# Optimization experiments

Measured on AMD Instinct MI355X. Metric: run time of the kernel, lower is better.

The kernel has to match this reference:

```python
import jax, jax.numpy as jnp
import numpy as np

N, D, H, E, K = 8192, 512, 2048, 8, 2  # tokens, input/output dim, hidden, experts, top-k
EPS = float(np.finfo(np.float64).eps)   # np.finfo(float).eps used by SparseDispatcher
NOISE_EPS = 1e-2                        # standard noisy-top-k gating epsilon


def setup_inputs() -> dict:
    key = jax.random.key(0)
    ks = jax.random.split(key, 8)
    s = 0.02  # weight scale to keep exp() in combine numerically sane
    return {
        "x": jax.random.normal(ks[0], (N, D), jnp.float32),
        "gate_feat": jax.random.normal(ks[1], (N, 2 * D), jnp.float32),
        "noise": jax.random.normal(ks[2], (N, E), jnp.float32),
        "w_gate": jax.random.normal(ks[3], (2 * D, E), jnp.float32) * s,
        "w_noise": jax.random.normal(ks[4], (2 * D, E), jnp.float32) * s,
        "fc1_w": jax.random.normal(ks[5], (E, H, D), jnp.float32) * s,
        "fc1_b": jnp.zeros((E, H), jnp.float32),
        "fc2_w": jax.random.normal(ks[6], (E, D, H), jnp.float32) * s,
        "fc2_b": jnp.zeros((E, D), jnp.float32),
    }


def reference(x, gate_feat, noise, w_gate, w_noise, fc1_w, fc1_b, fc2_w, fc2_b):
    # --- noisy top-k gating ---
    clean_logits = gate_feat @ w_gate                               # [N, E]
    noise_stddev = jax.nn.softplus(gate_feat @ w_noise) + NOISE_EPS  # [N, E]
    logits = clean_logits + noise * noise_stddev                    # randn_like * stddev
    top_vals, top_idx = jax.lax.top_k(logits, K + 1)                # top k+1 as in Shazeer gating
    top_k_gates = jax.nn.softmax(top_vals[:, :K], axis=-1)          # softmax over top-k logits
    gates = jnp.zeros_like(logits).at[jnp.arange(N)[:, None], top_idx[:, :K]].set(top_k_gates)

    # --- per-expert MLP (grouped GEMM; dense-masked form, math-equal to sparse dispatch
    # since zero-gate contributions vanish in the weighted combine) ---
    h = jax.nn.gelu(jnp.einsum('nd,ehd->enh', x, fc1_w) + fc1_b[:, None, :],
                    approximate=False)                              # torch nn.GELU = exact erf
    expert_out = jnp.einsum('enh,eoh->eno', h, fc2_w) + fc2_b[:, None, :]  # [E, N, D]

    # --- SparseDispatcher.combine: exp, gate-weight, scatter-add, eps-fill, log ---
    combined = jnp.einsum('ne,eno->no', gates, jnp.exp(expert_out))  # [N, D]
    combined = jnp.where(combined == 0, EPS, combined)
    return jnp.log(combined)
```

## Files before the change

kernel.cpp:

```cpp
#include <hip/hip_runtime.h>
#include <hip/hip_bf16.h>

#define NTOK 8192
#define DIM  512
#define HID  2048
#define NEXP 8
#define GFD  1024
#define NPAIR (NTOK*2)
#define EPSD 2.220446049250313e-16f

typedef __bf16 bf16;
typedef __bf16 bf16x4 __attribute__((ext_vector_type(4)));
typedef __bf16 bf16x8 __attribute__((ext_vector_type(8)));
typedef float  f32x4  __attribute__((ext_vector_type(4)));

__device__ __forceinline__ void cvt4(const float* __restrict__ src,
                                     bf16* __restrict__ dst, int i) {
    float4 v = ((const float4*)src)[i];
    bf16x4 o = { (bf16)v.x, (bf16)v.y, (bf16)v.z, (bf16)v.w };
    ((bf16x4*)dst)[i] = o;
}

__global__ __launch_bounds__(256) void convert_kernel(
    const float* __restrict__ x, const float* __restrict__ w1,
    const float* __restrict__ w2,
    bf16* __restrict__ xo, bf16* __restrict__ w1o, bf16* __restrict__ w2o)
{
    int tid = blockIdx.x * 256 + threadIdx.x;
    int stride = gridDim.x * 256;
    for (int i = tid; i < NTOK*DIM/4; i += stride)      cvt4(x,  xo,  i);
    for (int i = tid; i < NEXP*HID*DIM/4; i += stride)  cvt4(w1, w1o, i);
    for (int i = tid; i < NEXP*DIM*HID/4; i += stride)  cvt4(w2, w2o, i);
}

__global__ __launch_bounds__(256) void gate_gemm_kernel(
    const float* __restrict__ gf, const float* __restrict__ wg,
    const float* __restrict__ wn, float* __restrict__ partial)
{
    const int bt = blockIdx.x;
    const int bd = blockIdx.y;
    const int tid = threadIdx.x;

    __shared__ float sgf[128*129];
    __shared__ float sw[128][16];

    #pragma unroll
    for (int i = 0; i < 4; ++i) {
        int idx = i*256 + tid;
        sw[idx>>3][idx&7]     = wg[bd*1024 + idx];
        sw[idx>>3][8+(idx&7)] = wn[bd*1024 + idx];
    }
    const float4* gf4 = (const float4*)gf;
    #pragma unroll
    for (int i = 0; i < 16; ++i) {
        int c = i*256 + tid;
        int row = c >> 5, c4 = c & 31;
        float4 v = gf4[(size_t)(bt*128+row)*(GFD/4) + bd*32 + c4];
        float* dst = sgf + row*129 + c4*4;
        dst[0]=v.x; dst[1]=v.y; dst[2]=v.z; dst[3]=v.w;
    }
    __syncthreads();

    const int og = tid >> 6;
    const int lane = tid & 63;
    const int t0 = lane*2, t1 = t0+1;
    float a0=0,a1=0,a2=0,a3=0, b0=0,b1=0,b2=0,b3=0;
    #pragma unroll 4
    for (int dd = 0; dd < 128; ++dd) {
        float f0 = sgf[t0*129+dd];
        float f1 = sgf[t1*129+dd];
        float4 w = *(const float4*)&sw[dd][og*4];
        a0 += f0*w.x; a1 += f0*w.y; a2 += f0*w.z; a3 += f0*w.w;
        b0 += f1*w.x; b1 += f1*w.y; b2 += f1*w.z; b3 += f1*w.w;
    }
    size_t pbase = ((size_t)bd*NTOK + bt*128)*16 + og*4;
    *(float4*)&partial[pbase + (size_t)t0*16] = make_float4(a0,a1,a2,a3);
    *(float4*)&partial[pbase + (size_t)t1*16] = make_float4(b0,b1,b2,b3);
}

__global__ __launch_bounds__(256) void finalize_kernel(
    const float* __restrict__ partial, const float* __restrict__ noise,
    int* __restrict__ tok_e, float* __restrict__ tok_g, int* __restrict__ counts)
{
    __shared__ int hist[8];
    int tid = threadIdx.x;
    if (tid < 8) hist[tid] = 0;
    __syncthreads();
    int n = blockIdx.x*256 + tid;

    float lg[16];
    #pragma unroll
    for (int k = 0; k < 16; ++k) lg[k] = 0.f;
    #pragma unroll
    for (int j = 0; j < 8; ++j) {
        const float4* p = (const float4*)(partial + ((size_t)j*NTOK + n)*16);
        float4 q0 = p[0], q1 = p[1], q2 = p[2], q3 = p[3];
        lg[0]+=q0.x; lg[1]+=q0.y; lg[2]+=q0.z; lg[3]+=q0.w;
        lg[4]+=q1.x; lg[5]+=q1.y; lg[6]+=q1.z; lg[7]+=q1.w;
        lg[8]+=q2.x; lg[9]+=q2.y; lg[10]+=q2.z; lg[11]+=q2.w;
        lg[12]+=q3.x; lg[13]+=q3.y; lg[14]+=q3.z; lg[15]+=q3.w;
    }
    float v0=-1e30f, v1=-1e30f; int i0=0, i1=0;
    #pragma unroll
    for (int e = 0; e < 8; ++e) {
        float xn = lg[8+e];
        float sp = fmaxf(xn, 0.f) + log1pf(expf(-fabsf(xn)));
        float l = lg[e] + noise[(size_t)n*NEXP+e] * (sp + 1e-2f);
        if (l > v0)      { v1=v0; i1=i0; v0=l; i0=e; }
        else if (l > v1) { v1=l; i1=e; }
    }
    float g1 = expf(v1 - v0);
    float s  = 1.0f + g1;
    tok_e[n] = i0 | (i1 << 8);
    tok_g[2*n]   = 1.0f / s;
    tok_g[2*n+1] = g1 / s;
    atomicAdd(&hist[i0], 1);
    atomicAdd(&hist[i1], 1);
    __syncthreads();
    if (tid < 8) atomicAdd(&counts[tid], hist[tid]);
}

__global__ void scan_kernel(const int* __restrict__ counts,
                            int* __restrict__ offsets, int* __restrict__ cursors)
{
    if (threadIdx.x == 0) {
        int s = 0;
        for (int e = 0; e < NEXP; ++e) { offsets[e] = s; cursors[e] = s; s += counts[e]; }
        offsets[NEXP] = s;
    }
}

__global__ __launch_bounds__(256) void dispatch_kernel(
    const int* __restrict__ tok_e, const float* __restrict__ tok_g,
    int* __restrict__ cursors, int* __restrict__ pair_token, float* __restrict__ pair_gate,
    int* __restrict__ slot0, int* __restrict__ slot1)
{
    __shared__ int hist[8];
    __shared__ int base[8];
    int tid = threadIdx.x;
    if (tid < 8) hist[tid] = 0;
    __syncthreads();
    int n = blockIdx.x*256 + tid;
    int ee = tok_e[n];
    int e0 = ee & 255, e1 = (ee >> 8) & 255;
    atomicAdd(&hist[e0], 1);
    atomicAdd(&hist[e1], 1);
    __syncthreads();
    if (tid < 8) base[tid] = atomicAdd(&cursors[tid], hist[tid]);
    __syncthreads();
    int s0 = atomicAdd(&base[e0], 1);
    pair_token[s0] = n; pair_gate[s0] = tok_g[2*n];
    slot0[n] = s0;
    int s1 = atomicAdd(&base[e1], 1);
    pair_token[s1] = n; pair_gate[s1] = tok_g[2*n+1];
    slot1[n] = s1;
}

#define GLL16(gsrc, ldst) \
    __builtin_amdgcn_global_load_lds( \
        (__attribute__((address_space(1))) void*)(gsrc), \
        (__attribute__((address_space(3))) void*)(ldst), 16, 0, 0)

__global__ __launch_bounds__(256) void gemm1_kernel(
    const bf16* __restrict__ xb, const bf16* __restrict__ w1b,
    const float* __restrict__ fc1b,
    const int* __restrict__ pair_token, const int* __restrict__ offsets,
    bf16* __restrict__ hbuf)
{
    const int nt = blockIdx.x;
    const int mt = blockIdx.y;
    const int e  = blockIdx.z;
    const int seg0 = offsets[e], seg1 = offsets[e+1];
    const int cnt = seg1 - seg0;
    const int mbase = mt * 128;
    if (mbase >= cnt) return;

    __shared__ bf16 ldsA[128*64];
    __shared__ bf16 ldsB[128*64];

    const int tid = threadIdx.x;
    const int wid = tid >> 6;
    const int lane = tid & 63;
    const int wr = wid >> 1, wc = wid & 1;

    const bf16* srcA[4];
    const bf16* srcB[4];
    #pragma unroll
    for (int i = 0; i < 4; ++i) {
        int c = wid*256 + i*64 + lane;
        int r = c >> 3, c16 = c & 7;
        int sw = (c16 ^ (r & 7)) * 8;
        int p = seg0 + mbase + r;
        if (p > seg1 - 1) p = seg1 - 1;
        srcA[i] = xb + (size_t)pair_token[p] * DIM + sw;
        srcB[i] = w1b + ((size_t)e*HID + nt*128 + r) * DIM + sw;
    }

    f32x4 acc[4][4] = {};

    for (int kk = 0; kk < DIM; kk += 64) {
        #pragma unroll
        for (int i = 0; i < 4; ++i) {
            GLL16(srcA[i] + kk, (char*)ldsA + wid*4096 + i*1024);
            GLL16(srcB[i] + kk, (char*)ldsB + wid*4096 + i*1024);
        }
        __syncthreads();
        #pragma unroll
        for (int ks = 0; ks < 2; ++ks) {
            bf16x8 av[4], bv[4];
            #pragma unroll
            for (int m = 0; m < 4; ++m) {
                int row = wr*64 + m*16 + (lane & 15);
                int sw = (ks*4 + (lane >> 4)) ^ (row & 7);
                av[m] = *(const bf16x8*)(ldsA + row*64 + sw*8);
            }
            #pragma unroll
            for (int n = 0; n < 4; ++n) {
                int row = wc*64 + n*16 + (lane & 15);
                int sw = (ks*4 + (lane >> 4)) ^ (row & 7);
                bv[n] = *(const bf16x8*)(ldsB + row*64 + sw*8);
            }
            #pragma unroll
            for (int m = 0; m < 4; ++m)
                #pragma unroll
                for (int n = 0; n < 4; ++n)
                    acc[m][n] = __builtin_amdgcn_mfma_f32_16x16x32_bf16(
                        av[m], bv[n], acc[m][n], 0, 0, 0);
        }
        __syncthreads();
    }

    #pragma unroll
    for (int m = 0; m < 4; ++m) {
        #pragma unroll
        for (int jj = 0; jj < 4; ++jj) {
            int rt = wr*64 + m*16 + (lane >> 4)*4 + jj;
            int row = mbase + rt;
            if (row < cnt) {
                size_t hrow = (size_t)(seg0 + row) * HID;
                #pragma unroll
                for (int n = 0; n < 4; ++n) {
                    int col = nt*128 + wc*64 + n*16 + (lane & 15);
                    float v = acc[m][n][jj] + fc1b[e*HID + col];
                    float g = 0.5f * v * (1.0f + erff(v * 0.70710678118654752f));
                    hbuf[hrow + col] = (bf16)g;
                }
            }
        }
    }
}

__global__ __launch_bounds__(256) void gemm2_kernel(
    const bf16* __restrict__ hbuf, const bf16* __restrict__ w2b,
    const float* __restrict__ fc2b,
    const float* __restrict__ pair_gate,
    const int* __restrict__ offsets, bf16* __restrict__ pout)
{
    const int nt = blockIdx.x;
    const int mt = blockIdx.y;
    const int e  = blockIdx.z;
    const int seg0 = offsets[e], seg1 = offsets[e+1];
    const int cnt = seg1 - seg0;
    const int mbase = mt * 128;
    if (mbase >= cnt) return;

    __shared__ bf16 ldsA[128*64];
    __shared__ bf16 ldsB[128*64];

    const int tid = threadIdx.x;
    const int wid = tid >> 6;
    const int lane = tid & 63;
    const int wr = wid >> 1, wc = wid & 1;

    const bf16* srcA[4];
    const bf16* srcB[4];
    #pragma unroll
    for (int i = 0; i < 4; ++i) {
        int c = wid*256 + i*64 + lane;
        int r = c >> 3, c16 = c & 7;
        int sw = (c16 ^ (r & 7)) * 8;
        int p = seg0 + mbase + r;
        if (p > seg1 - 1) p = seg1 - 1;
        srcA[i] = hbuf + (size_t)p * HID + sw;
        srcB[i] = w2b + ((size_t)e*DIM + nt*128 + r) * HID + sw;
    }

    f32x4 acc[4][4] = {};

    for (int kk = 0; kk < HID; kk += 64) {
        #pragma unroll
        for (int i = 0; i < 4; ++i) {
            GLL16(srcA[i] + kk, (char*)ldsA + wid*4096 + i*1024);
            GLL16(srcB[i] + kk, (char*)ldsB + wid*4096 + i*1024);
        }
        __syncthreads();
        #pragma unroll
        for (int ks = 0; ks < 2; ++ks) {
            bf16x8 av[4], bv[4];
            #pragma unroll
            for (int m = 0; m < 4; ++m) {
                int row = wr*64 + m*16 + (lane & 15);
                int sw = (ks*4 + (lane >> 4)) ^ (row & 7);
                av[m] = *(const bf16x8*)(ldsA + row*64 + sw*8);
            }
            #pragma unroll
            for (int n = 0; n < 4; ++n) {
                int row = wc*64 + n*16 + (lane & 15);
                int sw = (ks*4 + (lane >> 4)) ^ (row & 7);
                bv[n] = *(const bf16x8*)(ldsB + row*64 + sw*8);
            }
            #pragma unroll
            for (int m = 0; m < 4; ++m)
                #pragma unroll
                for (int n = 0; n < 4; ++n)
                    acc[m][n] = __builtin_amdgcn_mfma_f32_16x16x32_bf16(
                        av[m], bv[n], acc[m][n], 0, 0, 0);
        }
        __syncthreads();
    }

    #pragma unroll
    for (int m = 0; m < 4; ++m) {
        #pragma unroll
        for (int jj = 0; jj < 4; ++jj) {
            int rt = wr*64 + m*16 + (lane >> 4)*4 + jj;
            int row = mbase + rt;
            if (row < cnt) {
                int p = seg0 + row;
                float gate = pair_gate[p];
                bf16* prow = pout + (size_t)p * DIM;
                #pragma unroll
                for (int n = 0; n < 4; ++n) {
                    int col = nt*128 + wc*64 + n*16 + (lane & 15);
                    float v = acc[m][n][jj] + fc2b[e*DIM + col];
                    prow[col] = (bf16)(gate * expf(v));
                }
            }
        }
    }
}

__global__ __launch_bounds__(256) void combine_kernel(
    const bf16* __restrict__ pout, const int* __restrict__ slot0,
    const int* __restrict__ slot1, float* __restrict__ out)
{
    const int wid = threadIdx.x >> 6;
    const int lane = threadIdx.x & 63;
    const int n = blockIdx.x*4 + wid;
    const int s0 = slot0[n], s1 = slot1[n];
    bf16x8 a = ((const bf16x8*)(pout + (size_t)s0 * DIM))[lane];
    bf16x8 b = ((const bf16x8*)(pout + (size_t)s1 * DIM))[lane];
    float4 r0, r1;
    float* orow = out + (size_t)n * DIM + lane*8;
    float c;
    c = (float)a[0] + (float)b[0]; r0.x = logf(c == 0.f ? EPSD : c);
    c = (float)a[1] + (float)b[1]; r0.y = logf(c == 0.f ? EPSD : c);
    c = (float)a[2] + (float)b[2]; r0.z = logf(c == 0.f ? EPSD : c);
    c = (float)a[3] + (float)b[3]; r0.w = logf(c == 0.f ? EPSD : c);
    c = (float)a[4] + (float)b[4]; r1.x = logf(c == 0.f ? EPSD : c);
    c = (float)a[5] + (float)b[5]; r1.y = logf(c == 0.f ? EPSD : c);
    c = (float)a[6] + (float)b[6]; r1.z = logf(c == 0.f ? EPSD : c);
    c = (float)a[7] + (float)b[7]; r1.w = logf(c == 0.f ? EPSD : c);
    ((float4*)orow)[0] = r0;
    ((float4*)orow)[1] = r1;
}

extern "C" void kernel_launch(void* const* d_in, const int* in_sizes, int n_in,
                              void* d_out, int out_size, void* d_ws, size_t ws_size,
                              hipStream_t stream)
{
    const float* x     = (const float*)d_in[0];
    const float* gf    = (const float*)d_in[1];
    const float* noise = (const float*)d_in[2];
    const float* wg    = (const float*)d_in[3];
    const float* wn    = (const float*)d_in[4];
    const float* fc1w  = (const float*)d_in[5];
    const float* fc1b  = (const float*)d_in[6];
    const float* fc2w  = (const float*)d_in[7];
    const float* fc2b  = (const float*)d_in[8];
    float* out = (float*)d_out;

    char* ws = (char*)d_ws;
    size_t off = 0;
    bf16* xb  = (bf16*)(ws + off); off += (size_t)NTOK*DIM*2;
    bf16* w1b = (bf16*)(ws + off); off += (size_t)NEXP*HID*DIM*2;
    bf16* w2b = (bf16*)(ws + off); off += (size_t)NEXP*DIM*HID*2;
    bf16* hb  = (bf16*)(ws + off); off += (size_t)NPAIR*HID*2;
    int*   pair_token = (int*)  (ws + off); off += (size_t)NPAIR*4;
    float* pair_gate  = (float*)(ws + off); off += (size_t)NPAIR*4;
    int*   tok_e      = (int*)  (ws + off); off += (size_t)NTOK*4;
    float* tok_g      = (float*)(ws + off); off += (size_t)NTOK*2*4;
    int*   slot0      = (int*)  (ws + off); off += (size_t)NTOK*4;
    int*   slot1      = (int*)  (ws + off); off += (size_t)NTOK*4;
    int*   counts     = (int*)  (ws + off); off += 64;
    int*   offsets    = (int*)  (ws + off); off += 64;
    int*   cursors    = (int*)  (ws + off); off += 64;
    if (ws_size < off) return;

    float* partial = (float*)hb;
    bf16* pout = (bf16*)ws;

    hipMemsetAsync(counts, 0, 32, stream);
    convert_kernel<<<2048, 256, 0, stream>>>(x, fc1w, fc2w, xb, w1b, w2b);
    gate_gemm_kernel<<<dim3(64, 8), 256, 0, stream>>>(gf, wg, wn, partial);
    finalize_kernel<<<NTOK/256, 256, 0, stream>>>(partial, noise, tok_e, tok_g, counts);
    scan_kernel<<<1, 64, 0, stream>>>(counts, offsets, cursors);
    dispatch_kernel<<<NTOK/256, 256, 0, stream>>>(tok_e, tok_g, cursors,
                                                  pair_token, pair_gate, slot0, slot1);
    gemm1_kernel<<<dim3(16, 64, 8), 256, 0, stream>>>(xb, w1b, fc1b, pair_token, offsets, hb);
    gemm2_kernel<<<dim3(4, 64, 8), 256, 0, stream>>>(hb, w2b, fc2b, pair_gate, offsets, pout);
    combine_kernel<<<NTOK/4, 256, 0, stream>>>(pout, slot0, slot1, out);
}
```

Before: 237.0 us.

## Use compact tile list for grouped GEMMs and widen gemm1 tiles to 128x256

The scan kernel now builds a compact list of (expert, m-tile) pairs, so both GEMMs launch a grid sized to the real tile count instead of 64 m-tiles per expert, most of which exited at once. gemm1 moves to 512 threads with a 128x256 output tile, so each staged A tile is reused across twice as many columns. MFMA sections are also wrapped in s_setprio. The risks are more LDS per block and lower occupancy in gemm1, and MAXTILES=136 is a fixed upper bound on the tile count.

Measured after the change: 197.5 us (median of 3 runs). 1.2x faster.

```diff
diff --git a/kernel.cpp b/kernel.cpp
--- a/kernel.cpp
+++ b/kernel.cpp
@@ -8,6 +8,7 @@
 #define GFD  1024
 #define NPAIR (NTOK*2)
 #define EPSD 2.220446049250313e-16f
+#define MAXTILES 136
 
 typedef __bf16 bf16;
 typedef __bf16 bf16x4 __attribute__((ext_vector_type(4)));
@@ -121,12 +122,19 @@
 }
 
 __global__ void scan_kernel(const int* __restrict__ counts,
-                            int* __restrict__ offsets, int* __restrict__ cursors)
+                            int* __restrict__ offsets, int* __restrict__ cursors,
+                            int* __restrict__ tlist, int* __restrict__ ntiles)
 {
     if (threadIdx.x == 0) {
-        int s = 0;
-        for (int e = 0; e < NEXP; ++e) { offsets[e] = s; cursors[e] = s; s += counts[e]; }
+        int s = 0, nt = 0;
+        for (int e = 0; e < NEXP; ++e) {
+            offsets[e] = s; cursors[e] = s;
+            int c = counts[e];
+            for (int mt = 0; mt*128 < c; ++mt) tlist[nt++] = e | (mt << 8);
+            s += c;
+        }
         offsets[NEXP] = s;
+        ntiles[0] = nt;
     }
 }
 
@@ -161,49 +169,59 @@
         (__attribute__((address_space(1))) void*)(gsrc), \
         (__attribute__((address_space(3))) void*)(ldst), 16, 0, 0)
 
-__global__ __launch_bounds__(256) void gemm1_kernel(
+__global__ __launch_bounds__(512) void gemm1_kernel(
     const bf16* __restrict__ xb, const bf16* __restrict__ w1b,
     const float* __restrict__ fc1b,
     const int* __restrict__ pair_token, const int* __restrict__ offsets,
+    const int* __restrict__ tlist, const int* __restrict__ ntiles,
     bf16* __restrict__ hbuf)
 {
-    const int nt = blockIdx.x;
-    const int mt = blockIdx.y;
-    const int e  = blockIdx.z;
+    const int ntp = blockIdx.x;
+    const int tix = blockIdx.y;
+    if (tix >= ntiles[0]) return;
+    const int code = tlist[tix];
+    const int e  = code & 255;
+    const int mt = code >> 8;
     const int seg0 = offsets[e], seg1 = offsets[e+1];
     const int cnt = seg1 - seg0;
     const int mbase = mt * 128;
-    if (mbase >= cnt) return;
 
     __shared__ bf16 ldsA[128*64];
-    __shared__ bf16 ldsB[128*64];
+    __shared__ bf16 ldsB[256*64];
 
     const int tid = threadIdx.x;
     const int wid = tid >> 6;
     const int lane = tid & 63;
-    const int wr = wid >> 1, wc = wid & 1;
-
-    const bf16* srcA[4];
+    const int wr = wid >> 2, wc = wid & 3;
+
+    const bf16* srcA[2];
     const bf16* srcB[4];
     #pragma unroll
-    for (int i = 0; i < 4; ++i) {
-        int c = wid*256 + i*64 + lane;
+    for (int i = 0; i < 2; ++i) {
+        int c = i*512 + tid;
         int r = c >> 3, c16 = c & 7;
         int sw = (c16 ^ (r & 7)) * 8;
         int p = seg0 + mbase + r;
         if (p > seg1 - 1) p = seg1 - 1;
         srcA[i] = xb + (size_t)pair_token[p] * DIM + sw;
-        srcB[i] = w1b + ((size_t)e*HID + nt*128 + r) * DIM + sw;
+    }
+    #pragma unroll
+    for (int i = 0; i < 4; ++i) {
+        int c = i*512 + tid;
+        int r = c >> 3, c16 = c & 7;
+        int sw = (c16 ^ (r & 7)) * 8;
+        srcB[i] = w1b + ((size_t)e*HID + ntp*256 + r) * DIM + sw;
     }
 
     f32x4 acc[4][4] = {};
 
     for (int kk = 0; kk < DIM; kk += 64) {
         #pragma unroll
-        for (int i = 0; i < 4; ++i) {
-            GLL16(srcA[i] + kk, (char*)ldsA + wid*4096 + i*1024);
-            GLL16(srcB[i] + kk, (char*)ldsB + wid*4096 + i*1024);
-        }
+        for (int i = 0; i < 2; ++i)
+            GLL16(srcA[i] + kk, (char*)ldsA + i*8192 + tid*16);
+        #pragma unroll
+        for (int i = 0; i < 4; ++i)
+            GLL16(srcB[i] + kk, (char*)ldsB + i*8192 + tid*16);
         __syncthreads();
         #pragma unroll
         for (int ks = 0; ks < 2; ++ks) {
@@ -220,12 +238,14 @@
                 int sw = (ks*4 + (lane >> 4)) ^ (row & 7);
                 bv[n] = *(const bf16x8*)(ldsB + row*64 + sw*8);
             }
+            __builtin_amdgcn_s_setprio(1);
             #pragma unroll
             for (int m = 0; m < 4; ++m)
                 #pragma unroll
                 for (int n = 0; n < 4; ++n)
                     acc[m][n] = __builtin_amdgcn_mfma_f32_16x16x32_bf16(
                         av[m], bv[n], acc[m][n], 0, 0, 0);
+            __builtin_amdgcn_s_setprio(0);
         }
         __syncthreads();
     }
@@ -240,7 +260,7 @@
                 size_t hrow = (size_t)(seg0 + row) * HID;
                 #pragma unroll
                 for (int n = 0; n < 4; ++n) {
-                    int col = nt*128 + wc*64 + n*16 + (lane & 15);
+                    int col = ntp*256 + wc*64 + n*16 + (lane & 15);
                     float v = acc[m][n][jj] + fc1b[e*HID + col];
                     float g = 0.5f * v * (1.0f + erff(v * 0.70710678118654752f));
                     hbuf[hrow + col] = (bf16)g;
@@ -254,15 +274,19 @@
     const bf16* __restrict__ hbuf, const bf16* __restrict__ w2b,
     const float* __restrict__ fc2b,
     const float* __restrict__ pair_gate,
-    const int* __restrict__ offsets, bf16* __restrict__ pout)
+    const int* __restrict__ offsets,
+    const int* __restrict__ tlist, const int* __restrict__ ntiles,
+    bf16* __restrict__ pout)
 {
     const int nt = blockIdx.x;
-    const int mt = blockIdx.y;
-    const int e  = blockIdx.z;
+    const int tix = blockIdx.y;
+    if (tix >= ntiles[0]) return;
+    const int code = tlist[tix];
+    const int e  = code & 255;
+    const int mt = code >> 8;
     const int seg0 = offsets[e], seg1 = offsets[e+1];
     const int cnt = seg1 - seg0;
     const int mbase = mt * 128;
-    if (mbase >= cnt) return;
 
     __shared__ bf16 ldsA[128*64];
     __shared__ bf16 ldsB[128*64];
@@ -309,12 +333,14 @@
                 int sw = (ks*4 + (lane >> 4)) ^ (row & 7);
                 bv[n] = *(const bf16x8*)(ldsB + row*64 + sw*8);
             }
+            __builtin_amdgcn_s_setprio(1);
             #pragma unroll
             for (int m = 0; m < 4; ++m)
                 #pragma unroll
                 for (int n = 0; n < 4; ++n)
                     acc[m][n] = __builtin_amdgcn_mfma_f32_16x16x32_bf16(
                         av[m], bv[n], acc[m][n], 0, 0, 0);
+            __builtin_amdgcn_s_setprio(0);
         }
         __syncthreads();
     }
@@ -395,6 +421,8 @@
     int*   counts     = (int*)  (ws + off); off += 64;
     int*   offsets    = (int*)  (ws + off); off += 64;
     int*   cursors    = (int*)  (ws + off); off += 64;
+    int*   tlist      = (int*)  (ws + off); off += MAXTILES*4;
+    int*   ntiles     = (int*)  (ws + off); off += 64;
     if (ws_size < off) return;
 
     float* partial = (float*)hb;
@@ -404,10 +432,12 @@
     convert_kernel<<<2048, 256, 0, stream>>>(x, fc1w, fc2w, xb, w1b, w2b);
     gate_gemm_kernel<<<dim3(64, 8), 256, 0, stream>>>(gf, wg, wn, partial);
     finalize_kernel<<<NTOK/256, 256, 0, stream>>>(partial, noise, tok_e, tok_g, counts);
-    scan_kernel<<<1, 64, 0, stream>>>(counts, offsets, cursors);
+    scan_kernel<<<1, 64, 0, stream>>>(counts, offsets, cursors, tlist, ntiles);
     dispatch_kernel<<<NTOK/256, 256, 0, stream>>>(tok_e, tok_g, cursors,
                                                   pair_token, pair_gate, slot0, slot1);
-    gemm1_kernel<<<dim3(16, 64, 8), 256, 0, stream>>>(xb, w1b, fc1b, pair_token, offsets, hb);
-    gemm2_kernel<<<dim3(4, 64, 8), 256, 0, stream>>>(hb, w2b, fc2b, pair_gate, offsets, pout);
+    gemm1_kernel<<<dim3(8, MAXTILES), 512, 0, stream>>>(xb, w1b, fc1b, pair_token, offsets,
+                                                        tlist, ntiles, hb);
+    gemm2_kernel<<<dim3(4, MAXTILES), 256, 0, stream>>>(hb, w2b, fc2b, pair_gate, offsets,
+                                                        tlist, ntiles, pout);
     combine_kernel<<<NTOK/4, 256, 0, stream>>>(pout, slot0, slot1, out);
 }
```
